# Performance work log

Measured on AMD Instinct MI355X. Metric: run time of the kernel, lower is better.

## Reference

```python
import jax, jax.numpy as jnp
import numpy as np

TEMPERATURE = 1.0
MIN_DISP = 0.1


def setup_inputs() -> dict:
    key = jax.random.key(0)
    k1, = jax.random.split(key, 1)
    B, V, C, H, W = 4, 2, 128, 128, 512
    feat = jax.random.normal(k1, (B, V, C, H, W), dtype=jnp.float32)
    # normalized intrinsics (fx < 50 triggers normalized_intri branch)
    K = jnp.array([[0.8, 0.0, 0.5], [0.0, 0.8, 0.5], [0.0, 0.0, 1.0]], dtype=jnp.float32)
    intri = jnp.broadcast_to(K, (B, V, 3, 3))
    # extrinsics: left = identity, right = identity translated by baseline 0.1 in x
    eye = jnp.eye(4, dtype=jnp.float32)
    lext = jnp.broadcast_to(eye, (B, 4, 4))
    rext = eye.at[0, 3].set(0.1)
    rext = jnp.broadcast_to(rext, (B, 4, 4))
    extri = jnp.stack([lext, rext], axis=1)
    near = jnp.full((B, V), 0.1, dtype=jnp.float32)
    far = jnp.full((B, V), 10.0, dtype=jnp.float32)
    return {"feat": feat, "extri": extri, "intri": intri, "near": near, "far": far}


def reference(feat, extri, intri, near, far):
    B, V, C, H, W = feat.shape
    lfeat, rfeat = feat[:, 0], feat[:, 1]          # (B,C,H,W)
    lintri = intri[:, 0]
    lextri, rextri = extri[:, 0], extri[:, 1]
    lfar = far[:, 0]

    # dot-product cost volume, groups G=1: (B,1,H,W1,W2)
    vol = jnp.einsum('bchi,bchj->bhij', lfeat, rfeat) / np.sqrt(C)
    vol = vol[:, None]

    # triangular geometry mask (left image first -> tril), applied AFTER softmax
    mask = jnp.tril(jnp.ones((W, W), dtype=vol.dtype))
    idx = jnp.arange(W, dtype=vol.dtype)
    prob = jax.nn.softmax(vol / TEMPERATURE, axis=-1) * mask

    # soft-argmax correspondence and confidence
    corresp = jnp.sum(prob * idx, axis=-1)         # (B,1,H,W)
    conf = jnp.max(prob, axis=-1)                  # (B,1,H,W)

    # correspondence -> normalized disparity -> depth
    disp = jnp.abs(corresp - idx) / W
    disp = jnp.maximum(disp, MIN_DISP)
    fx = lintri[:, 0, 0][:, None, None, None]
    baseline = jnp.linalg.norm(lextri[:, :3, 3] - rextri[:, :3, 3], axis=-1)
    depth = fx * baseline[:, None, None, None] / disp

    # depth_type == 'norm_depth'
    depth_conversed = depth / lfar[:, None, None, None]

    out = jnp.concatenate((depth_conversed, conf), axis=1)[:, None]  # (B,1,2,H,W)
    return out
```

## Files before the change

kernel.cpp:

```cpp
#include <hip/hip_runtime.h>

typedef _Float16 f16x8 __attribute__((ext_vector_type(8)));
typedef float    f32x4 __attribute__((ext_vector_type(4)));

#define C_DIM 128
#define H_DIM 128
#define W_DIM 512
#define CH_STRIDE 65536
#define V_STRIDE  8388608
#define SJ 32
#define NSTRIP 16
#define ROW_H 136

__global__ __launch_bounds__(512, 4) void costvol_kernel(
    const float* __restrict__ feat,
    const float* __restrict__ extri,
    const float* __restrict__ intri,
    const float* __restrict__ farp,
    float* __restrict__ out)
{
    __shared__ _Float16 Bs[2][SJ][ROW_H];

    const int tid  = threadIdx.x;
    const int wave = tid >> 6;
    const int lane = tid & 63;
    const int l15  = lane & 15;
    const int l4   = lane >> 4;

    const int bid   = blockIdx.x;
    const int lb    = (bid & 7) * 128 + (bid >> 3);
    const int bh    = lb >> 1;
    const int ihalf = lb & 1;
    const int b  = bh >> 7;
    const int h  = bh & 127;
    const int rowbase = ihalf * 256 + wave * 32;

    const float* lbase = feat + (size_t)(b * 2) * V_STRIDE + (size_t)h * W_DIM;
    const float* rbase = lbase + V_STRIDE;

    const int jj = tid & 31;
    const int c0 = (tid >> 5) * 8;

    float br[8];

#define ISSUE(s) do {                                                       \
    const float* bp_ = rbase + (size_t)((s) * SJ + jj);                     \
    _Pragma("unroll")                                                       \
    for (int d_ = 0; d_ < 8; ++d_)                                          \
        br[d_] = bp_[(size_t)(c0 + d_) * CH_STRIDE];                        \
} while (0)

#define STAGE(bf) do {                                                      \
    f16x8 w_;                                                               \
    _Pragma("unroll")                                                       \
    for (int d_ = 0; d_ < 8; ++d_) w_[d_] = (_Float16)br[d_];               \
    *(f16x8*)&Bs[bf][jj][c0] = w_;                                          \
} while (0)

    ISSUE(0);
    __builtin_amdgcn_sched_barrier(0);

    f16x8 a[2][4];
    const float kScale = 0.08838834764831845f;
    #pragma unroll
    for (int ks = 0; ks < 4; ++ks) {
        #pragma unroll
        for (int fi = 0; fi < 2; ++fi) {
            const float* p = lbase + (size_t)(ks * 32 + l4 * 8) * CH_STRIDE
                             + (size_t)(rowbase + fi * 16 + l15);
            f16x8 f;
            #pragma unroll
            for (int e = 0; e < 8; ++e)
                f[e] = (_Float16)(p[(size_t)e * CH_STRIDE] * kScale);
            a[fi][ks] = f;
        }
        __builtin_amdgcn_sched_barrier(0);
    }

    STAGE(0);
    __syncthreads();

    float Zp[8], Mp[8], Wp[8];
    #pragma unroll
    for (int s2 = 0; s2 < 8; ++s2) { Zp[s2] = 0.f; Mp[s2] = 0.f; Wp[s2] = 0.f; }

#define COMPUTE(bf, s) do {                                                  \
    f32x4 acc[2][2];                                                         \
    _Pragma("unroll")                                                        \
    for (int fi = 0; fi < 2; ++fi) {                                         \
        acc[fi][0] = (f32x4){0.f, 0.f, 0.f, 0.f};                            \
        acc[fi][1] = (f32x4){0.f, 0.f, 0.f, 0.f};                            \
    }                                                                        \
    __builtin_amdgcn_s_setprio(1);                                           \
    _Pragma("unroll")                                                        \
    for (int ks = 0; ks < 4; ++ks) {                                         \
        f16x8 b0 = *(const f16x8*)&Bs[bf][l15][ks * 32 + l4 * 8];            \
        f16x8 b1 = *(const f16x8*)&Bs[bf][16 + l15][ks * 32 + l4 * 8];       \
        _Pragma("unroll")                                                    \
        for (int fi = 0; fi < 2; ++fi) {                                     \
            acc[fi][0] = __builtin_amdgcn_mfma_f32_16x16x32_f16(a[fi][ks], b0, acc[fi][0], 0, 0, 0); \
            acc[fi][1] = __builtin_amdgcn_mfma_f32_16x16x32_f16(a[fi][ks], b1, acc[fi][1], 0, 0, 0); \
        }                                                                    \
    }                                                                        \
    __builtin_amdgcn_s_setprio(0);                                           \
    const int jbase_ = (s) * SJ;                                             \
    _Pragma("unroll")                                                        \
    for (int fi = 0; fi < 2; ++fi) {                                         \
        const int ti0 = rowbase + fi * 16;                                   \
        _Pragma("unroll")                                                    \
        for (int fj = 0; fj < 2; ++fj) {                                     \
            const int tj = jbase_ + fj * 16;                                 \
            const float jf = (float)(tj + l15);                              \
            if (tj + 15 <= ti0) {                     \
                _Pragma("unroll")                                            \
                for (int r = 0; r < 4; ++r) {                                \
                    const int sl = fi * 4 + r;                               \
                    float e = __expf(acc[fi][fj][r]);                        \
                    Zp[sl] += e;                                             \
                    Mp[sl] = fmaxf(Mp[sl], e);                               \
                    Wp[sl] += jf * e;                                        \
                }                                                            \
            } else if (tj > ti0 + 15) {                    \
                _Pragma("unroll")                                            \
                for (int r = 0; r < 4; ++r) {                                \
                    float e = __expf(acc[fi][fj][r]);                        \
                    Zp[fi * 4 + r] += e;                                     \
                }                                                            \
            } else {                                      \
                _Pragma("unroll")                                            \
                for (int r = 0; r < 4; ++r) {                                \
                    const int sl = fi * 4 + r;                               \
                    float e = __expf(acc[fi][fj][r]);                        \
                    Zp[sl] += e;                                             \
                    const int irow = ti0 + l4 * 4 + r;                       \
                    float em = ((tj + l15) <= irow) ? e : 0.f;               \
                    Mp[sl] = fmaxf(Mp[sl], em);                              \
                    Wp[sl] += jf * em;                                       \
                }                                                            \
            }                                                                \
        }                                                                    \
    }                                                                        \
} while (0)

    int buf = 0;
    #pragma unroll 1
    for (int s = 0; s < NSTRIP; ++s) {
        if (s + 1 < NSTRIP) ISSUE(s + 1);
        __builtin_amdgcn_sched_barrier(0);
        COMPUTE(buf, s);
        if (s + 1 < NSTRIP) STAGE(buf ^ 1);
        __syncthreads();
        buf ^= 1;
    }

    #pragma unroll
    for (int m = 1; m <= 8; m <<= 1) {
        #pragma unroll
        for (int sl = 0; sl < 8; ++sl) {
            Zp[sl] += __shfl_xor(Zp[sl], m, 64);
            Wp[sl] += __shfl_xor(Wp[sl], m, 64);
            Mp[sl] = fmaxf(Mp[sl], __shfl_xor(Mp[sl], m, 64));
        }
    }

    if (l15 == 0) {
        const float fx = intri[b * 18];
        const float dx = extri[b * 32 + 3]  - extri[b * 32 + 19];
        const float dy = extri[b * 32 + 7]  - extri[b * 32 + 23];
        const float dz = extri[b * 32 + 11] - extri[b * 32 + 27];
        const float bl = sqrtf(dx * dx + dy * dy + dz * dz);
        const float lfar = farp[b * 2];
        const float kd = fx * bl / lfar;
        #pragma unroll
        for (int sl = 0; sl < 8; ++sl) {
            const int fi = sl >> 2, r = sl & 3;
            const int irow = rowbase + fi * 16 + l4 * 4 + r;
            const float Z = Zp[sl];
            const float conf = Mp[sl] / Z;
            const float corr = Wp[sl] / Z;
            float disp = fabsf(corr - (float)irow) * (1.0f / 512.0f);
            disp = fmaxf(disp, 0.1f);
            out[(size_t)(b * 2 + 0) * CH_STRIDE + h * W_DIM + irow] = kd / disp;
            out[(size_t)(b * 2 + 1) * CH_STRIDE + h * W_DIM + irow] = conf;
        }
    }
#undef ISSUE
#undef STAGE
#undef COMPUTE
}

extern "C" void kernel_launch(void* const* d_in, const int* in_sizes, int n_in,
                              void* d_out, int out_size, void* d_ws, size_t ws_size,
                              hipStream_t stream) {
    const float* feat  = (const float*)d_in[0];
    const float* extri = (const float*)d_in[1];
    const float* intri = (const float*)d_in[2];
    const float* farp  = (const float*)d_in[4];
    float* out = (float*)d_out;
    costvol_kernel<<<dim3(1024), dim3(512), 0, stream>>>(feat, extri, intri, farp, out);
}
```

Measured before the change: 77.80 us.

## Deepen right-feature prefetch to two strips ahead and fold log2e into scale

Right-image loads now go through two register sets and are issued two strips ahead, so global load latency is hidden behind two compute phases instead of one. The loop is unrolled by two with fixed LDS buffer indices. The log2(e) factor is folded into the left-feature scale so the exponential becomes exp2f. The LDS row pitch changes from 136 to 160 halves, which alters the bank mapping. The extra prefetch registers raise VGPR pressure under the 4-waves launch bound.

```diff
diff --git a/kernel.cpp b/kernel.cpp
--- a/kernel.cpp
+++ b/kernel.cpp
@@ -10,7 +10,7 @@
 #define V_STRIDE  8388608
 #define SJ 32
 #define NSTRIP 16
-#define ROW_H 136
+#define ROW_H 160
 
 __global__ __launch_bounds__(512, 4) void costvol_kernel(
     const float* __restrict__ feat,
@@ -41,27 +41,28 @@
     const int jj = tid & 31;
     const int c0 = (tid >> 5) * 8;
 
-    float br[8];
-
-#define ISSUE(s) do {                                                       \
+    float brA[8], brB[8];
+
+#define ISSUE(br, s) do {                                                   \
     const float* bp_ = rbase + (size_t)((s) * SJ + jj);                     \
     _Pragma("unroll")                                                       \
     for (int d_ = 0; d_ < 8; ++d_)                                          \
-        br[d_] = bp_[(size_t)(c0 + d_) * CH_STRIDE];                        \
+        (br)[d_] = bp_[(size_t)(c0 + d_) * CH_STRIDE];                      \
 } while (0)
 
-#define STAGE(bf) do {                                                      \
+#define STAGE(br, bf) do {                                                  \
     f16x8 w_;                                                               \
     _Pragma("unroll")                                                       \
-    for (int d_ = 0; d_ < 8; ++d_) w_[d_] = (_Float16)br[d_];               \
+    for (int d_ = 0; d_ < 8; ++d_) w_[d_] = (_Float16)(br)[d_];             \
     *(f16x8*)&Bs[bf][jj][c0] = w_;                                          \
 } while (0)
 
-    ISSUE(0);
+    ISSUE(brA, 0);
+    ISSUE(brB, 1);
     __builtin_amdgcn_sched_barrier(0);
 
     f16x8 a[2][4];
-    const float kScale = 0.08838834764831845f;
+    const float kScale = 0.08838834764831845f * 1.44269504088896340f;
     #pragma unroll
     for (int ks = 0; ks < 4; ++ks) {
         #pragma unroll
@@ -77,7 +78,7 @@
         __builtin_amdgcn_sched_barrier(0);
     }
 
-    STAGE(0);
+    STAGE(brA, 0);
     __syncthreads();
 
     float Zp[8], Mp[8], Wp[8];
@@ -115,7 +116,7 @@
                 _Pragma("unroll")                                            \
                 for (int r = 0; r < 4; ++r) {                                \
                     const int sl = fi * 4 + r;                               \
-                    float e = __expf(acc[fi][fj][r]);                        \
+                    float e = exp2f(acc[fi][fj][r]);                         \
                     Zp[sl] += e;                                             \
                     Mp[sl] = fmaxf(Mp[sl], e);                               \
                     Wp[sl] += jf * e;                                        \
@@ -123,14 +124,14 @@
             } else if (tj > ti0 + 15) {                    \
                 _Pragma("unroll")                                            \
                 for (int r = 0; r < 4; ++r) {                                \
-                    float e = __expf(acc[fi][fj][r]);                        \
+                    float e = exp2f(acc[fi][fj][r]);                         \
                     Zp[fi * 4 + r] += e;                                     \
                 }                                                            \
             } else {                                      \
                 _Pragma("unroll")                                            \
                 for (int r = 0; r < 4; ++r) {                                \
                     const int sl = fi * 4 + r;                               \
-                    float e = __expf(acc[fi][fj][r]);                        \
+                    float e = exp2f(acc[fi][fj][r]);                         \
                     Zp[sl] += e;                                             \
                     const int irow = ti0 + l4 * 4 + r;                       \
                     float em = ((tj + l15) <= irow) ? e : 0.f;               \
@@ -142,15 +143,19 @@
     }                                                                        \
 } while (0)
 
-    int buf = 0;
     #pragma unroll 1
-    for (int s = 0; s < NSTRIP; ++s) {
-        if (s + 1 < NSTRIP) ISSUE(s + 1);
+    for (int s = 0; s < NSTRIP; s += 2) {
+        if (s + 2 < NSTRIP) ISSUE(brA, s + 2);
         __builtin_amdgcn_sched_barrier(0);
-        COMPUTE(buf, s);
-        if (s + 1 < NSTRIP) STAGE(buf ^ 1);
+        COMPUTE(0, s);
+        STAGE(brB, 1);
         __syncthreads();
-        buf ^= 1;
+
+        if (s + 3 < NSTRIP) ISSUE(brB, s + 3);
+        __builtin_amdgcn_sched_barrier(0);
+        COMPUTE(1, s + 1);
+        if (s + 2 < NSTRIP) STAGE(brA, 0);
+        __syncthreads();
     }
 
     #pragma unroll
```

Result: slower. 89.43 us (+14.9%).
